# Kernel tuning notes

Hardware: AMD Instinct MI355X
Metric: run time of the kernel (lower is better)

Reference implementation:

```python
import jax, jax.numpy as jnp
import numpy as np

# Level-7 icosphere: nv vertices, nf faces
NV, NF = 163842, 327680
IN_C, NECK_C, OUT_C, B = 64, 32, 128, 2
EPS = 1e-5


def setup_inputs() -> dict:
    key = jax.random.key(0)
    ks = jax.random.split(key, 16)
    f32 = jnp.float32
    d = {}
    d['x'] = jax.random.normal(ks[0], (B, IN_C, NV), f32)
    # conv1 (1x1), bn1
    d['w1'] = jax.random.normal(ks[1], (NECK_C, IN_C), f32) * 0.05
    d['b1'] = jnp.zeros((NECK_C,), f32)
    d['gamma1'] = jnp.ones((NECK_C,), f32); d['beta1'] = jnp.zeros((NECK_C,), f32)
    # MeshConv: coeffs (out,in,4 taps: id, lap, grad_ew, grad_ns) + bias
    d['coeffs'] = jax.random.normal(ks[2], (NECK_C, NECK_C, 4), f32) * 0.05
    d['mc_bias'] = jnp.zeros((NECK_C,), f32)
    d['gamma2'] = jnp.ones((NECK_C,), f32); d['beta2'] = jnp.zeros((NECK_C,), f32)
    # conv3 (1x1), bn3
    d['w3'] = jax.random.normal(ks[3], (OUT_C, NECK_C), f32) * 0.05
    d['b3'] = jnp.zeros((OUT_C,), f32)
    d['gamma3'] = jnp.ones((OUT_C,), f32); d['beta3'] = jnp.zeros((OUT_C,), f32)
    # shortcut conv_ + bn_ (diff_chan since in!=out)
    d['wsc'] = jax.random.normal(ks[4], (OUT_C, IN_C), f32) * 0.05
    d['bsc'] = jnp.zeros((OUT_C,), f32)
    d['gammasc'] = jnp.ones((OUT_C,), f32); d['betasc'] = jnp.zeros((OUT_C,), f32)
    # sparse mesh operators (gather indices + values):
    # G: face gradient, 3 components per face from 3 face vertices
    d['idx_G'] = jax.random.randint(ks[5], (NF, 3), 0, NV, jnp.int32)
    d['vals_G'] = jax.random.normal(ks[6], (NF, 3, 3), f32) * 0.1
    # EW/NS tangent direction per face (3-vectors)
    d['EW'] = jax.random.normal(ks[7], (NF, 3), f32)
    d['NS'] = jax.random.normal(ks[8], (NF, 3), f32)
    # L: vertex laplacian, ~7 nnz per row
    d['idx_L'] = jax.random.randint(ks[9], (NV, 7), 0, NV, jnp.int32)
    d['vals_L'] = jax.random.normal(ks[10], (NV, 7), f32) * 0.1
    # F2V: face-to-vertex averaging, ~6 faces per vertex
    d['idx_F2V'] = jax.random.randint(ks[11], (NV, 6), 0, NF, jnp.int32)
    d['vals_F2V'] = jax.random.uniform(ks[12], (NV, 6), f32) / 6.0
    return d


def _bn(x, g, b):
    # training-mode BatchNorm1d over (batch, spatial), per channel
    m = x.mean(axis=(0, 2), keepdims=True)
    v = ((x - m) ** 2).mean(axis=(0, 2), keepdims=True)
    return g[None, :, None] * (x - m) * jax.lax.rsqrt(v + EPS) + b[None, :, None]


def _conv1x1(x, w, b):
    return jnp.einsum('oc,bcn->bon', w, x) + b[None, :, None]


def _mesh_conv(x, coeffs, bias, idx_G, vals_G, EW, NS, idx_L, vals_L, idx_F2V, vals_F2V):
    # laplacian: sparse matmul via gather  (B,C,NV)
    lap = jnp.einsum('bcnk,nk->bcn', x[:, :, idx_L], vals_L)
    # face gradient: (B,C,NF,3 components)
    grad_face = jnp.einsum('bcfj,fij->bcfi', x[:, :, idx_G], vals_G)
    g_ew = jnp.einsum('bcfi,fi->bcf', grad_face, EW)
    g_ns = jnp.einsum('bcfi,fi->bcf', grad_face, NS)
    # face -> vertex averaging
    gv_ew = jnp.einsum('bcnk,nk->bcn', g_ew[:, :, idx_F2V], vals_F2V)
    gv_ns = jnp.einsum('bcnk,nk->bcn', g_ns[:, :, idx_F2V], vals_F2V)
    feat = jnp.stack([x, lap, gv_ew, gv_ns], axis=-1)  # (B,C,NV,4)
    return jnp.einsum('bcnk,ock->bon', feat, coeffs) + bias[None, :, None]


def reference(x, w1, b1, gamma1, beta1, coeffs, mc_bias, gamma2, beta2,
              w3, b3, gamma3, beta3, wsc, bsc, gammasc, betasc,
              idx_G, vals_G, EW, NS, idx_L, vals_L, idx_F2V, vals_F2V):
    # shortcut branch (diff_chan)
    x2 = _bn(_conv1x1(x, wsc, bsc), gammasc, betasc)
    # main branch
    h = jax.nn.relu(_bn(_conv1x1(x, w1, b1), gamma1, beta1))
    h = _mesh_conv(h, coeffs, mc_bias, idx_G, vals_G, EW, NS, idx_L, vals_L, idx_F2V, vals_F2V)
    h = jax.nn.relu(_bn(h, gamma2, beta2))
    h = _bn(_conv1x1(h, w3, b3), gamma3, beta3)
    return jax.nn.relu(h + x2)
```

## Files before the change

kernel.cpp:

```cpp
#include <hip/hip_runtime.h>

#define NV   163842
#define NF   327680
#define BB   2
#define INC  64
#define NECK 32
#define OUTC 128
#define NT   (BB*NV)
#define EPSB 1e-5f

typedef unsigned short ushort_t;
typedef __attribute__((ext_vector_type(8))) short bf16x8;
typedef __attribute__((ext_vector_type(4))) float f32x4;

#define F_SX8  0
#define F_SS8  512
#define F_A1   33280
#define F_C1   33312
#define F_ASC  33344
#define F_CSC  33472
#define F_S2S  33600
#define F_S2Q  33632
#define F_A2   33664
#define F_C2   33696
#define F_SHR  33728
#define F_SS2  33760
#define F_A3   34784
#define F_C3   34912
#define F_CF   35040
#define STATN  35168
#define F_W1B  35200
#define F_CFB  36224
#define F_Y1   38272
#define F_H2   (F_Y1 + NT*16)
#define F_I18  (F_H2 + NT*16)
#define F_WEW  (F_I18 + NV*18)
#define F_WNS  (F_WEW + NV*18)
#define F_XB   (F_WNS + NV*18)

#define FSTR 136

__device__ __forceinline__ float bf2f(ushort_t u) {
    union { unsigned int i; float f; } x; x.i = ((unsigned int)u) << 16; return x.f;
}
__device__ __forceinline__ ushort_t f2bf(float f) {
    union { float f; unsigned int i; } x; x.f = f;
    unsigned int r = x.i + 0x7fffu + ((x.i >> 16) & 1u);
    return (ushort_t)(r >> 16);
}

__global__ __launch_bounds__(256) void k_xcvt(const float* __restrict__ x,
                                              float* __restrict__ ws,
                                              ushort_t* __restrict__ xb) {
    __shared__ float SSl[64 * 68 + 64];
    const int tid = threadIdx.x;
    const int w = tid >> 6, l = tid & 63;
    const int o16 = l & 15, kg = l >> 4;

    for (int i = tid; i < 64 * 68 + 64; i += 256) SSl[i] = 0.f;
    __syncthreads();

    f32x4 acc[10];
#pragma unroll
    for (int i = 0; i < 10; ++i) acc[i] = (f32x4){0.f, 0.f, 0.f, 0.f};
    f32x4 accS[4];
#pragma unroll
    for (int i = 0; i < 4; ++i) accS[i] = (f32x4){0.f, 0.f, 0.f, 0.f};

    bf16x8 onesf;
    {
        short ov = (o16 == 0) ? (short)0x3F80 : (short)0;
#pragma unroll
        for (int j = 0; j < 8; ++j) onesf[j] = ov;
    }

    const int NCHB = (NV + 63) >> 6;
    const int NW = gridDim.x * 4;
    for (int cid = blockIdx.x * 4 + w; cid < 2 * NCHB; cid += NW) {
        const int b = (cid >= NCHB) ? 1 : 0;
        const int tc = cid - b * NCHB;
        const int n0 = tc << 6;
        const float* xsrc = x + (size_t)b * 64 * NV;
        const bool full = (n0 + 64 <= NV);
        const int n = n0 + l;
        if (n < NV) {
            unsigned int pk[32];
#pragma unroll
            for (int c2 = 0; c2 < 32; ++c2) {
                float f0 = xsrc[(size_t)(2 * c2) * NV + n];
                float f1 = xsrc[(size_t)(2 * c2 + 1) * NV + n];
                pk[c2] = (unsigned int)f2bf(f0) | ((unsigned int)f2bf(f1) << 16);
            }
            ushort_t* row = xb + (size_t)(b * NV + n) * 64;
#pragma unroll
            for (int j = 0; j < 8; ++j) {
                uint4 q = make_uint4(pk[4 * j], pk[4 * j + 1], pk[4 * j + 2], pk[4 * j + 3]);
                *(uint4*)(row + j * 8) = q;
            }
        }
        bf16x8 fr[4][2];
#pragma unroll
        for (int mt = 0; mt < 4; ++mt) {
            const float* rp = xsrc + (size_t)(mt * 16 + o16) * NV + n0;
#pragma unroll
            for (int ks = 0; ks < 2; ++ks) {
                const int v0 = ks * 32 + kg * 8;
                float f[8];
                if (full) {
                    float4 q0 = *(const float4*)(rp + v0);
                    float4 q1 = *(const float4*)(rp + v0 + 4);
                    f[0] = q0.x; f[1] = q0.y; f[2] = q0.z; f[3] = q0.w;
                    f[4] = q1.x; f[5] = q1.y; f[6] = q1.z; f[7] = q1.w;
                } else {
#pragma unroll
                    for (int j = 0; j < 8; ++j)
                        f[j] = (n0 + v0 + j < NV) ? rp[v0 + j] : 0.f;
                }
                bf16x8 fb;
#pragma unroll
                for (int j = 0; j < 8; ++j) fb[j] = (short)f2bf(f[j]);
                fr[mt][ks] = fb;
            }
        }
#pragma unroll
        for (int ks = 0; ks < 2; ++ks) {
            int tt = 0;
#pragma unroll
            for (int mt = 0; mt < 4; ++mt) {
#pragma unroll
                for (int nt2 = 0; nt2 < 4; ++nt2) {
                    if (nt2 >= mt) {
                        acc[tt] = __builtin_amdgcn_mfma_f32_16x16x32_bf16(fr[mt][ks], fr[nt2][ks], acc[tt], 0, 0, 0);
                        ++tt;
                    }
                }
                accS[mt] = __builtin_amdgcn_mfma_f32_16x16x32_bf16(onesf, fr[mt][ks], accS[mt], 0, 0, 0);
            }
        }
    }
    {
        int tt = 0;
#pragma unroll
        for (int mt = 0; mt < 4; ++mt) {
#pragma unroll
            for (int nt2 = 0; nt2 < 4; ++nt2) {
                if (nt2 >= mt) {
#pragma unroll
                    for (int r = 0; r < 4; ++r) {
                        const int row = mt * 16 + kg * 4 + r;
                        const int col = nt2 * 16 + o16;
                        atomicAdd(&SSl[row * 68 + col], acc[tt][r]);
                    }
                    ++tt;
                }
            }
            if (kg == 0) atomicAdd(&SSl[64 * 68 + mt * 16 + o16], accS[mt][0]);
        }
    }
    __syncthreads();
    {
        float* SSg = ws + F_SS8 + (size_t)(blockIdx.x & 7) * 4096;
        for (int i = tid; i < 64 * 64; i += 256) {
            const int r = i >> 6, c = i & 63;
            if (c >= r) {
                float v = SSl[r * 68 + c];
                if (v != 0.f) atomicAdd(&SSg[r * 64 + c], v);
            }
        }
        if (tid < 64) atomicAdd(&ws[F_SX8 + (blockIdx.x & 7) * 64 + tid], SSl[64 * 68 + tid]);
    }
}

__global__ __launch_bounds__(256) void k_fold1(const float* __restrict__ w1,
                                               const float* __restrict__ g1,
                                               const float* __restrict__ be1,
                                               const float* __restrict__ wsc,
                                               const float* __restrict__ gsc,
                                               const float* __restrict__ besc,
                                               float* __restrict__ ws,
                                               ushort_t* __restrict__ w1b) {
    __shared__ float SSl[4096];
    __shared__ float Sxl[64];
    const int tid = threadIdx.x;
    for (int i = tid; i < 4096; i += 256) {
        const int r = i >> 6, c = i & 63;
        float v = 0.f;
        if (c >= r) {
#pragma unroll
            for (int s = 0; s < 8; ++s) v += ws[F_SS8 + s * 4096 + i];
        }
        SSl[i] = v;
    }
    if (tid < 64) {
        float v = 0.f;
#pragma unroll
        for (int s = 0; s < 8; ++s) v += ws[F_SX8 + s * 64 + tid];
        Sxl[tid] = v;
    }
    __syncthreads();
    for (int i = tid; i < 4096; i += 256) {
        const int r = i >> 6, c = i & 63;
        if (c < r) SSl[i] = SSl[c * 64 + r];
    }
    __syncthreads();
    if (tid >= 32) return;
    const int bk = blockIdx.x;
    const float* w;
    float gamma, beta;
    float *pa, *pc;
    if (bk == 0) {
        w = w1 + tid * 64; gamma = g1[tid]; beta = be1[tid];
        pa = ws + F_A1 + tid; pc = ws + F_C1 + tid;
    } else {
        int o = (bk - 1) * 32 + tid;
        w = wsc + o * 64; gamma = gsc[o]; beta = besc[o];
        pa = ws + F_ASC + o; pc = ws + F_CSC + o;
    }
    float4 wr[16];
#pragma unroll
    for (int i = 0; i < 16; ++i) wr[i] = *(const float4*)(w + i * 4);
    float dotm = 0.f, quad = 0.f;
#pragma unroll
    for (int i4 = 0; i4 < 16; ++i4) {
        float4 wi = wr[i4];
        float rd[4] = {0.f, 0.f, 0.f, 0.f};
#pragma unroll
        for (int j4 = 0; j4 < 16; ++j4) {
            float4 wj = wr[j4];
#pragma unroll
            for (int r = 0; r < 4; ++r) {
                const float* row = &SSl[(i4 * 4 + r) * 64 + j4 * 4];
                rd[r] += row[0] * wj.x + row[1] * wj.y + row[2] * wj.z + row[3] * wj.w;
            }
        }
        dotm += wi.x * Sxl[i4 * 4] + wi.y * Sxl[i4 * 4 + 1] + wi.z * Sxl[i4 * 4 + 2] + wi.w * Sxl[i4 * 4 + 3];
        quad += wi.x * rd[0] + wi.y * rd[1] + wi.z * rd[2] + wi.w * rd[3];
    }
    const float invN = 1.0f / (float)NT;
    const float mean0 = dotm * invN;
    const float var = quad * invN - mean0 * mean0;
    const float a = gamma * rsqrtf(var + EPSB);
    *pa = a;
    *pc = beta - a * mean0;
    if (bk == 0) {
#pragma unroll
        for (int i4 = 0; i4 < 16; ++i4) {
            w1b[tid * 64 + i4 * 4 + 0] = f2bf(a * wr[i4].x);
            w1b[tid * 64 + i4 * 4 + 1] = f2bf(a * wr[i4].y);
            w1b[tid * 64 + i4 * 4 + 2] = f2bf(a * wr[i4].z);
            w1b[tid * 64 + i4 * 4 + 3] = f2bf(a * wr[i4].w);
        }
    }
}

__global__ __launch_bounds__(256) void k_conv1(const ushort_t* __restrict__ xb,
                                               const ushort_t* __restrict__ w1b,
                                               const float* __restrict__ ws,
                                               ushort_t* __restrict__ y1) {
    const int tid = threadIdx.x;
    const int w = tid >> 6, l = tid & 63;
    const int o16 = l & 15, kg = l >> 4;
    bf16x8 af[2][2];
#pragma unroll
    for (int mt = 0; mt < 2; ++mt)
#pragma unroll
        for (int ks = 0; ks < 2; ++ks)
            af[mt][ks] = *(const bf16x8*)(w1b + (mt * 16 + o16) * 64 + ks * 32 + kg * 8);
    float c1r[2][4];
#pragma unroll
    for (int mt = 0; mt < 2; ++mt)
#pragma unroll
        for (int r = 0; r < 4; ++r)
            c1r[mt][r] = ws[F_C1 + mt * 16 + kg * 4 + r];

    const int NCH = (NT + 63) >> 6;
    for (int ch = blockIdx.x * 4 + w; ch < NCH; ch += gridDim.x * 4) {
        const int n0 = ch << 6;
        bf16x8 bf[4][2];
#pragma unroll
        for (int nt = 0; nt < 4; ++nt) {
            int row = n0 + nt * 16 + o16;
            row = row < NT ? row : NT - 1;
#pragma unroll
            for (int ks = 0; ks < 2; ++ks)
                bf[nt][ks] = *(const bf16x8*)(xb + (size_t)row * 64 + ks * 32 + kg * 8);
        }
        f32x4 acc[2][4];
#pragma unroll
        for (int mt = 0; mt < 2; ++mt)
#pragma unroll
            for (int nt = 0; nt < 4; ++nt) acc[mt][nt] = (f32x4){0.f, 0.f, 0.f, 0.f};
#pragma unroll
        for (int mt = 0; mt < 2; ++mt)
#pragma unroll
            for (int nt = 0; nt < 4; ++nt)
#pragma unroll
                for (int ks = 0; ks < 2; ++ks)
                    acc[mt][nt] = __builtin_amdgcn_mfma_f32_16x16x32_bf16(af[mt][ks], bf[nt][ks], acc[mt][nt], 0, 0, 0);
#pragma unroll
        for (int nt = 0; nt < 4; ++nt) {
            const int vert = n0 + nt * 16 + o16;
            if (vert < NT) {
#pragma unroll
                for (int mt = 0; mt < 2; ++mt) {
                    uint2 p;
                    p.x = (unsigned)f2bf(fmaxf(acc[mt][nt][0] + c1r[mt][0], 0.f)) |
                          ((unsigned)f2bf(fmaxf(acc[mt][nt][1] + c1r[mt][1], 0.f)) << 16);
                    p.y = (unsigned)f2bf(fmaxf(acc[mt][nt][2] + c1r[mt][2], 0.f)) |
                          ((unsigned)f2bf(fmaxf(acc[mt][nt][3] + c1r[mt][3], 0.f)) << 16);
                    *(uint2*)(y1 + (size_t)vert * 32 + mt * 16 + kg * 4) = p;
                }
            }
        }
    }
}

__global__ __launch_bounds__(256) void k_w18(const int* __restrict__ idx_F2V,
                                             const float* __restrict__ vals_F2V,
                                             const int* __restrict__ idx_G,
                                             const float* __restrict__ vals_G,
                                             const float* __restrict__ EW,
                                             const float* __restrict__ NS,
                                             int* __restrict__ i18,
                                             float* __restrict__ wew,
                                             float* __restrict__ wns) {
    const int n = blockIdx.x * 256 + threadIdx.x;
    if (n >= NV) return;
#pragma unroll
    for (int k = 0; k < 6; ++k) {
        int f = idx_F2V[n * 6 + k];
        float fv = vals_F2V[n * 6 + k];
        float e0 = EW[f * 3], e1 = EW[f * 3 + 1], e2 = EW[f * 3 + 2];
        float s0 = NS[f * 3], s1 = NS[f * 3 + 1], s2 = NS[f * 3 + 2];
#pragma unroll
        for (int j = 0; j < 3; ++j) {
            float g0 = vals_G[f * 9 + j], g1 = vals_G[f * 9 + 3 + j], g2 = vals_G[f * 9 + 6 + j];
            i18[n * 18 + k * 3 + j] = idx_G[f * 3 + j];
            wew[n * 18 + k * 3 + j] = fv * (g0 * e0 + g1 * e1 + g2 * e2);
            wns[n * 18 + k * 3 + j] = fv * (g0 * s0 + g1 * s1 + g2 * s2);
        }
    }
}

__global__ __launch_bounds__(256) void k_cvtcoef(const float* __restrict__ c,
                                                 ushort_t* __restrict__ cb) {
    int i = blockIdx.x * 256 + threadIdx.x;
    if (i < 4096) cb[i] = f2bf(c[i]);
}

__global__ __launch_bounds__(256, 3) void k_meshconv(const ushort_t* __restrict__ y1,
                                                     const ushort_t* __restrict__ cfb,
                                                     const int* __restrict__ idx_L,
                                                     const float* __restrict__ vals_L,
                                                     const int* __restrict__ i18,
                                                     const float* __restrict__ w18ew,
                                                     const float* __restrict__ w18ns,
                                                     ushort_t* __restrict__ h2,
                                                     float* __restrict__ ws) {
    __shared__ __align__(16) ushort_t feat[4][32 * FSTR];
    __shared__ float sred[64];
    const int tid = threadIdx.x;
    const int w = __builtin_amdgcn_readfirstlane(tid >> 6);
    const int lane = tid & 63;
    ushort_t* fw = &feat[w][0];
    const int bh = lane >> 5;
    const int c = lane & 31;
    const int ybase = bh * (NV * 32);
    const int o16 = lane & 15;
    const int kg = lane >> 4;

    if (tid < 64) sred[tid] = 0.f;
    __syncthreads();

    float ssum[8], sssq[8];
#pragma unroll
    for (int i = 0; i < 8; ++i) { ssum[i] = 0.f; sssq[i] = 0.f; }

    const int gw = blockIdx.x * 4 + w;
    const int NW = gridDim.x * 4;
    const int NCH = (NV + 15) >> 4;

    for (int ch = gw; ch < NCH; ch += NW) {
        const int n0 = ch << 4;
        for (int g = 0; g < 16; ++g) {
            const int n = n0 + g;
            const bool ok = (n < NV);
            const int nn = ok ? n : (NV - 1);
            float fx = bf2f(y1[ybase + (nn << 5) + c]);
            float lap = 0.f, gew = 0.f, gns = 0.f;
            const int* ilp = idx_L + nn * 7;
            const float* vlp = vals_L + nn * 7;
#pragma unroll
            for (int j = 0; j < 7; ++j) {
                int vi = ilp[j];
                float wv = vlp[j];
                lap += wv * bf2f(y1[ybase + (vi << 5) + c]);
            }
            const int* igp = i18 + nn * 18;
            const float* wep = w18ew + nn * 18;
            const float* wnp = w18ns + nn * 18;
#pragma unroll
            for (int j = 0; j < 18; ++j) {
                int vi = igp[j];
                float we = wep[j], wn = wnp[j];
                float v = bf2f(y1[ybase + (vi << 5) + c]);
                gew += we * v;
                gns += wn * v;
            }
            if (!ok) { fx = 0.f; lap = 0.f; gew = 0.f; gns = 0.f; }
            unsigned int lo = (unsigned int)f2bf(fx) | ((unsigned int)f2bf(lap) << 16);
            unsigned int hi = (unsigned int)f2bf(gew) | ((unsigned int)f2bf(gns) << 16);
            const int inst = bh * 16 + g;
            *(uint2*)(fw + inst * FSTR + (c << 2)) = make_uint2(lo, hi);
        }
        f32x4 acc[2][2];
#pragma unroll
        for (int mt = 0; mt < 2; ++mt)
#pragma unroll
            for (int nt = 0; nt < 2; ++nt) acc[mt][nt] = (f32x4){0.f, 0.f, 0.f, 0.f};
        bf16x8 bfr[2][4];
#pragma unroll
        for (int nt = 0; nt < 2; ++nt)
#pragma unroll
            for (int kt = 0; kt < 4; ++kt)
                bfr[nt][kt] = *(const bf16x8*)(fw + (nt * 16 + o16) * FSTR + kt * 32 + kg * 8);
#pragma unroll
        for (int mt = 0; mt < 2; ++mt) {
#pragma unroll
            for (int kt = 0; kt < 4; ++kt) {
                bf16x8 af = *(const bf16x8*)(cfb + (mt * 16 + o16) * 128 + kt * 32 + kg * 8);
                acc[mt][0] = __builtin_amdgcn_mfma_f32_16x16x32_bf16(af, bfr[0][kt], acc[mt][0], 0, 0, 0);
                acc[mt][1] = __builtin_amdgcn_mfma_f32_16x16x32_bf16(af, bfr[1][kt], acc[mt][1], 0, 0, 0);
            }
        }
        const int n = n0 + o16;
        if (n < NV) {
#pragma unroll
            for (int nt = 0; nt < 2; ++nt) {
                const int rowb = ((nt * NV + n) << 5);
#pragma unroll
                for (int mt = 0; mt < 2; ++mt) {
#pragma unroll
                    for (int r = 0; r < 4; ++r) {
                        float v = acc[mt][nt][r];
                        int o = mt * 16 + kg * 4 + r;
                        h2[rowb + o] = f2bf(v);
                        ssum[mt * 4 + r] += v;
                        sssq[mt * 4 + r] += v * v;
                    }
                }
            }
        }
    }

#pragma unroll
    for (int si = 0; si < 8; ++si) {
#pragma unroll
        for (int m = 1; m < 16; m <<= 1) {
            ssum[si] += __shfl_xor(ssum[si], m, 16);
            sssq[si] += __shfl_xor(sssq[si], m, 16);
        }
    }
    if (o16 == 0) {
#pragma unroll
        for (int mt = 0; mt < 2; ++mt)
#pragma unroll
            for (int r = 0; r < 4; ++r) {
                int o = mt * 16 + kg * 4 + r;
                atomicAdd(&sred[o], ssum[mt * 4 + r]);
                atomicAdd(&sred[32 + o], sssq[mt * 4 + r]);
            }
    }
    __syncthreads();
    if (tid < 64) atomicAdd(&ws[F_S2S + tid], sred[tid]);
}

__global__ void k_fold2(const float* __restrict__ g2, const float* __restrict__ be2,
                        float* __restrict__ ws) {
    const int c = threadIdx.x;
    if (c < 32) {
        const float invN = 1.0f / (float)NT;
        float m = ws[F_S2S + c] * invN;
        float var = ws[F_S2Q + c] * invN - m * m;
        float a = g2[c] * rsqrtf(var + EPSB);
        ws[F_A2 + c] = a;
        ws[F_C2 + c] = be2[c] - a * m;
    }
}

__global__ __launch_bounds__(256) void k_hrmoments(const ushort_t* __restrict__ h2,
                                                   float* __restrict__ ws) {
    __shared__ __align__(16) ushort_t tile[4][32 * 40];
    __shared__ float red[1056];
    const int tid = threadIdx.x;
    const int w = tid >> 6, l = tid & 63;
    ushort_t* T = &tile[w][0];
    const int c8 = (l & 3) * 8;
    const int v0 = l >> 2;
    const int fr = l & 15, kg = l >> 4;

    for (int i = tid; i < 1056; i += 256) red[i] = 0.f;
    __syncthreads();

    float a2r[8], c2r[8];
#pragma unroll
    for (int j = 0; j < 8; ++j) { a2r[j] = ws[F_A2 + c8 + j]; c2r[j] = ws[F_C2 + c8 + j]; }

    f32x4 acc[2][2];
#pragma unroll
    for (int a = 0; a < 2; ++a)
#pragma unroll
        for (int b = 0; b < 2; ++b) acc[a][b] = (f32x4){0.f, 0.f, 0.f, 0.f};
    float ssum[8];
#pragma unroll
    for (int j = 0; j < 8; ++j) ssum[j] = 0.f;

    const int NCH = (NT + 31) >> 5;
    for (int ch = blockIdx.x * 4 + w; ch < NCH; ch += gridDim.x * 4) {
        const int s0 = ch << 5;
#pragma unroll
        for (int i = 0; i < 2; ++i) {
            const int vert = i * 16 + v0;
            const int s = s0 + vert;
            uint4 q = make_uint4(0u, 0u, 0u, 0u);
            const bool ok = (s < NT);
            if (ok) q = *(const uint4*)(h2 + (size_t)s * 32 + c8);
            const ushort_t* qs = (const ushort_t*)&q;
            ushort_t hb[8];
#pragma unroll
            for (int j = 0; j < 8; ++j) {
                float hv = ok ? fmaxf(a2r[j] * bf2f(qs[j]) + c2r[j], 0.f) : 0.f;
                ssum[j] += hv;
                hb[j] = f2bf(hv);
            }
#pragma unroll
            for (int j = 0; j < 8; ++j) T[(c8 + j) * 40 + vert] = hb[j];
        }
        bf16x8 f0 = *(const bf16x8*)(T + fr * 40 + kg * 8);
        bf16x8 f1 = *(const bf16x8*)(T + (16 + fr) * 40 + kg * 8);
        acc[0][0] = __builtin_amdgcn_mfma_f32_16x16x32_bf16(f0, f0, acc[0][0], 0, 0, 0);
        acc[0][1] = __builtin_amdgcn_mfma_f32_16x16x32_bf16(f0, f1, acc[0][1], 0, 0, 0);
        acc[1][0] = __builtin_amdgcn_mfma_f32_16x16x32_bf16(f1, f0, acc[1][0], 0, 0, 0);
        acc[1][1] = __builtin_amdgcn_mfma_f32_16x16x32_bf16(f1, f1, acc[1][1], 0, 0, 0);
    }
#pragma unroll
    for (int mt = 0; mt < 2; ++mt)
#pragma unroll
        for (int nt = 0; nt < 2; ++nt)
#pragma unroll
            for (int r = 0; r < 4; ++r)
                atomicAdd(&red[(mt * 16 + kg * 4 + r) * 32 + nt * 16 + fr], acc[mt][nt][r]);
#pragma unroll
    for (int j = 0; j < 8; ++j) {
        float s = ssum[j];
        s += __shfl_xor(s, 4); s += __shfl_xor(s, 8);
        s += __shfl_xor(s, 16); s += __shfl_xor(s, 32);
        if (v0 == 0) atomicAdd(&red[1024 + c8 + j], s);
    }
    __syncthreads();
    for (int i = tid; i < 1024; i += 256) atomicAdd(&ws[F_SS2 + i], red[i]);
    if (tid < 32) atomicAdd(&ws[F_SHR + tid], red[1024 + tid]);
}

__global__ __launch_bounds__(128) void k_fold3(const float* __restrict__ w3,
                                               const float* __restrict__ wsc,
                                               const float* __restrict__ g3,
                                               const float* __restrict__ be3,
                                               float* __restrict__ ws,
                                               ushort_t* __restrict__ wfb) {
    __shared__ float SSl[1024];
    __shared__ float Sl[32];
    const int tid = threadIdx.x;
    for (int i = tid; i < 1024; i += 128) SSl[i] = ws[F_SS2 + i];
    if (tid < 32) Sl[tid] = ws[F_SHR + tid];
    __syncthreads();
    const int o = tid;
    float4 wr[8];
#pragma unroll
    for (int i = 0; i < 8; ++i) wr[i] = *(const float4*)(w3 + o * 32 + i * 4);
    float dotm = 0.f, quad = 0.f;
#pragma unroll
    for (int i4 = 0; i4 < 8; ++i4) {
        float4 wi = wr[i4];
        float rd[4] = {0.f, 0.f, 0.f, 0.f};
#pragma unroll
        for (int j4 = 0; j4 < 8; ++j4) {
            float4 wj = wr[j4];
#pragma unroll
            for (int r = 0; r < 4; ++r) {
                const float* row = &SSl[(i4 * 4 + r) * 32 + j4 * 4];
                rd[r] += row[0] * wj.x + row[1] * wj.y + row[2] * wj.z + row[3] * wj.w;
            }
        }
        dotm += wi.x * Sl[i4 * 4] + wi.y * Sl[i4 * 4 + 1] + wi.z * Sl[i4 * 4 + 2] + wi.w * Sl[i4 * 4 + 3];
        quad += wi.x * rd[0] + wi.y * rd[1] + wi.z * rd[2] + wi.w * rd[3];
    }
    const float invN = 1.0f / (float)NT;
    const float mean0 = dotm * invN;
    const float var = quad * invN - mean0 * mean0;
    const float a = g3[o] * rsqrtf(var + EPSB);
    const float cbias = be3[o] - a * mean0;
    ws[F_A3 + o] = a;
    ws[F_C3 + o] = cbias;
    const float asc = ws[F_ASC + o], csc = ws[F_CSC + o];
    ws[F_CF + o] = cbias + csc;
#pragma unroll
    for (int i4 = 0; i4 < 8; ++i4) {
        wfb[o * 96 + i4 * 4 + 0] = f2bf(a * wr[i4].x);
        wfb[o * 96 + i4 * 4 + 1] = f2bf(a * wr[i4].y);
        wfb[o * 96 + i4 * 4 + 2] = f2bf(a * wr[i4].z);
        wfb[o * 96 + i4 * 4 + 3] = f2bf(a * wr[i4].w);
    }
    for (int j = 0; j < 64; ++j)
        wfb[o * 96 + 32 + j] = f2bf(asc * wsc[o * 64 + j]);
}

__global__ __launch_bounds__(256) void k_final(const ushort_t* __restrict__ xb,
                                               const ushort_t* __restrict__ h2,
                                               const ushort_t* __restrict__ wfb,
                                               const float* __restrict__ ws,
                                               float* __restrict__ out) {
    __shared__ __align__(16) ushort_t feat[32 * 104];
    __shared__ __align__(16) float ol[128][33];
    const int tid = threadIdx.x;
    const int w = tid >> 6, l = tid & 63;
    const int fr = l & 15, kg = l >> 4;

    bf16x8 af[2][3];
#pragma unroll
    for (int mt = 0; mt < 2; ++mt)
#pragma unroll
        for (int kt = 0; kt < 3; ++kt)
            af[mt][kt] = *(const bf16x8*)(wfb + (w * 32 + mt * 16 + fr) * 96 + kt * 32 + kg * 8);
    float cfr[2][4];
#pragma unroll
    for (int mt = 0; mt < 2; ++mt)
#pragma unroll
        for (int r = 0; r < 4; ++r)
            cfr[mt][r] = ws[F_CF + w * 32 + mt * 16 + kg * 4 + r];

    const int hv = tid >> 3, hc4 = (tid & 7) * 4;
    float a2r[4], c2r[4];
#pragma unroll
    for (int j = 0; j < 4; ++j) { a2r[j] = ws[F_A2 + hc4 + j]; c2r[j] = ws[F_C2 + hc4 + j]; }
    const int xv = tid >> 3, xseg = tid & 7;
    const int oo = tid >> 1, ohalf = tid & 1;

    const int NCHK = (NV + 31) >> 5;
    for (int cid = blockIdx.x; cid < 2 * NCHK; cid += gridDim.x) {
        const int b = (cid >= NCHK) ? 1 : 0;
        const int t = cid - b * NCHK;
        const int n0 = t << 5;
        const int rem = NV - n0 < 32 ? NV - n0 : 32;
        {
            const int s = b * NV + n0 + hv;
            const bool ok = (hv < rem);
            uint2 q = make_uint2(0u, 0u);
            if (ok) q = *(const uint2*)(h2 + (size_t)s * 32 + hc4);
            const ushort_t* qs = (const ushort_t*)&q;
            unsigned int p0 = 0u, p1 = 0u;
            if (ok) {
                float h0 = fmaxf(a2r[0] * bf2f(qs[0]) + c2r[0], 0.f);
                float h1 = fmaxf(a2r[1] * bf2f(qs[1]) + c2r[1], 0.f);
                float h2v = fmaxf(a2r[2] * bf2f(qs[2]) + c2r[2], 0.f);
                float h3 = fmaxf(a2r[3] * bf2f(qs[3]) + c2r[3], 0.f);
                p0 = (unsigned int)f2bf(h0) | ((unsigned int)f2bf(h1) << 16);
                p1 = (unsigned int)f2bf(h2v) | ((unsigned int)f2bf(h3) << 16);
            }
            *(uint2*)(feat + hv * 104 + hc4) = make_uint2(p0, p1);
        }
        {
            const int s = b * NV + n0 + xv;
            uint4 q = make_uint4(0u, 0u, 0u, 0u);
            if (xv < rem) q = *(const uint4*)(xb + (size_t)s * 64 + xseg * 8);
            *(uint4*)(feat + xv * 104 + 32 + xseg * 8) = q;
        }
        __syncthreads();
        bf16x8 bf[2][3];
#pragma unroll
        for (int nt = 0; nt < 2; ++nt)
#pragma unroll
            for (int kt = 0; kt < 3; ++kt)
                bf[nt][kt] = *(const bf16x8*)(feat + (nt * 16 + fr) * 104 + kt * 32 + kg * 8);
        f32x4 acc[2][2];
#pragma unroll
        for (int mt = 0; mt < 2; ++mt)
#pragma unroll
            for (int nt = 0; nt < 2; ++nt) acc[mt][nt] = (f32x4){0.f, 0.f, 0.f, 0.f};
#pragma unroll
        for (int mt = 0; mt < 2; ++mt)
#pragma unroll
            for (int nt = 0; nt < 2; ++nt)
#pragma unroll
                for (int kt = 0; kt < 3; ++kt)
                    acc[mt][nt] = __builtin_amdgcn_mfma_f32_16x16x32_bf16(af[mt][kt], bf[nt][kt], acc[mt][nt], 0, 0, 0);
#pragma unroll
        for (int mt = 0; mt < 2; ++mt)
#pragma unroll
            for (int nt = 0; nt < 2; ++nt)
#pragma unroll
                for (int r = 0; r < 4; ++r)
                    ol[w * 32 + mt * 16 + kg * 4 + r][nt * 16 + fr] =
                        fmaxf(acc[mt][nt][r] + cfr[mt][r], 0.f);
        __syncthreads();
        {
            float* po = out + (size_t)(b * 128 + oo) * NV + n0 + ohalf * 16;
            if (rem == 32) {
#pragma unroll
                for (int j2 = 0; j2 < 8; ++j2)
                    *(float2*)(po + j2 * 2) = make_float2(ol[oo][ohalf * 16 + j2 * 2],
                                                         ol[oo][ohalf * 16 + j2 * 2 + 1]);
            } else {
#pragma unroll
                for (int j = 0; j < 16; ++j) {
                    int v = ohalf * 16 + j;
                    if (v < rem) po[j] = ol[oo][v];
                }
            }
        }
        __syncthreads();
    }
}

extern "C" void kernel_launch(void* const* d_in, const int* in_sizes, int n_in,
                              void* d_out, int out_size, void* d_ws, size_t ws_size,
                              hipStream_t stream) {
    (void)in_sizes; (void)n_in; (void)out_size; (void)ws_size;
    const float* x        = (const float*)d_in[0];
    const float* w1       = (const float*)d_in[1];
    const float* g1       = (const float*)d_in[3];
    const float* be1      = (const float*)d_in[4];
    const float* coeffs   = (const float*)d_in[5];
    const float* g2       = (const float*)d_in[7];
    const float* be2      = (const float*)d_in[8];
    const float* w3       = (const float*)d_in[9];
    const float* g3       = (const float*)d_in[11];
    const float* be3      = (const float*)d_in[12];
    const float* wsc      = (const float*)d_in[13];
    const float* gsc      = (const float*)d_in[15];
    const float* besc     = (const float*)d_in[16];
    const int*   idx_G    = (const int*)d_in[17];
    const float* vals_G   = (const float*)d_in[18];
    const float* EW       = (const float*)d_in[19];
    const float* NS       = (const float*)d_in[20];
    const int*   idx_L    = (const int*)d_in[21];
    const float* vals_L   = (const float*)d_in[22];
    const int*   idx_F2V  = (const int*)d_in[23];
    const float* vals_F2V = (const float*)d_in[24];
    float* ws  = (float*)d_ws;
    float* out = (float*)d_out;

    ushort_t* w1b = (ushort_t*)(ws + F_W1B);
    ushort_t* cfb = (ushort_t*)(ws + F_CFB);
    ushort_t* y1  = (ushort_t*)(ws + F_Y1);
    ushort_t* h2  = (ushort_t*)(ws + F_H2);
    ushort_t* xb  = (ushort_t*)(ws + F_XB);
    ushort_t* wfb = (ushort_t*)(ws + F_Y1);

    hipMemsetAsync(ws, 0, STATN * sizeof(float), stream);
    hipLaunchKernelGGL(k_xcvt, dim3(1280), dim3(256), 0, stream, x, ws, xb);
    hipLaunchKernelGGL(k_w18, dim3((NV + 255) / 256), dim3(256), 0, stream,
                       idx_F2V, vals_F2V, idx_G, vals_G, EW, NS,
                       (int*)(ws + F_I18), ws + F_WEW, ws + F_WNS);
    hipLaunchKernelGGL(k_cvtcoef, dim3(16), dim3(256), 0, stream, coeffs, cfb);
    hipLaunchKernelGGL(k_fold1, dim3(5), dim3(256), 0, stream, w1, g1, be1, wsc, gsc, besc, ws, w1b);
    hipLaunchKernelGGL(k_conv1, dim3(1280), dim3(256), 0, stream, xb, w1b, ws, y1);
    hipLaunchKernelGGL(k_meshconv, dim3(768), dim3(256), 0, stream,
                       y1, cfb, idx_L, vals_L,
                       (const int*)(ws + F_I18), ws + F_WEW, ws + F_WNS,
                       h2, ws);
    hipLaunchKernelGGL(k_fold2, dim3(1), dim3(32), 0, stream, g2, be2, ws);
    hipLaunchKernelGGL(k_hrmoments, dim3(1024), dim3(256), 0, stream, h2, ws);
    hipLaunchKernelGGL(k_fold3, dim3(1), dim3(128), 0, stream, w3, wsc, g3, be3, ws, wfb);
    hipLaunchKernelGGL(k_final, dim3(2048), dim3(256), 0, stream, xb, h2, wfb, ws, out);
}
```

Measured before the change: 552.7 us.

## Gather two channels per lane and two vertices per wave in meshconv

The meshconv gather loop now has each lane load a 32-bit pair of bf16 channels, with the two half-waves handling two different vertices at once. This halves the number of gather iterations per chunk and the number of load instructions issued. Launch bounds are raised to 4 blocks/SM and the grid is grown to 1024 blocks to add occupancy. In exchange each lane holds more accumulators and loads index/weight data for both vertices, which raises register pressure and redundant scalar loads.

```diff
diff --git a/kernel.cpp b/kernel.cpp
--- a/kernel.cpp
+++ b/kernel.cpp
@@ -348,7 +348,7 @@
     if (i < 4096) cb[i] = f2bf(c[i]);
 }
 
-__global__ __launch_bounds__(256, 3) void k_meshconv(const ushort_t* __restrict__ y1,
+__global__ __launch_bounds__(256, 4) void k_meshconv(const ushort_t* __restrict__ y1,
                                                      const ushort_t* __restrict__ cfb,
                                                      const int* __restrict__ idx_L,
                                                      const float* __restrict__ vals_L,
@@ -363,8 +363,9 @@
     const int w = __builtin_amdgcn_readfirstlane(tid >> 6);
     const int lane = tid & 63;
     ushort_t* fw = &feat[w][0];
-    const int bh = lane >> 5;
-    const int c = lane & 31;
+    const int gh = lane >> 5;
+    const int bh = (lane >> 4) & 1;
+    const int c2 = lane & 15;
     const int ybase = bh * (NV * 32);
     const int o16 = lane & 15;
     const int kg = lane >> 4;
@@ -382,36 +383,58 @@
 
     for (int ch = gw; ch < NCH; ch += NW) {
         const int n0 = ch << 4;
-        for (int g = 0; g < 16; ++g) {
-            const int n = n0 + g;
+        for (int jj = 0; jj < 8; ++jj) {
+            const int gA = 2 * jj;
+            const int nA = n0 + gA;
+            const int nB = nA + 1;
+            const int nnA = (nA < NV) ? nA : NV - 1;
+            const int nnB = (nB < NV) ? nB : NV - 1;
+            const int n = n0 + gA + gh;
             const bool ok = (n < NV);
-            const int nn = ok ? n : (NV - 1);
-            float fx = bf2f(y1[ybase + (nn << 5) + c]);
-            float lap = 0.f, gew = 0.f, gns = 0.f;
-            const int* ilp = idx_L + nn * 7;
-            const float* vlp = vals_L + nn * 7;
+            const int nn = gh ? nnB : nnA;
+            const ushort_t* yb = y1 + ybase;
+            unsigned int qs = *(const unsigned int*)(yb + (nn << 5) + (c2 << 1));
+            float fx0 = bf2f((ushort_t)(qs & 0xffffu));
+            float fx1 = bf2f((ushort_t)(qs >> 16));
+            float lap0 = 0.f, lap1 = 0.f, ge0 = 0.f, ge1 = 0.f, gn0 = 0.f, gn1 = 0.f;
 #pragma unroll
             for (int j = 0; j < 7; ++j) {
-                int vi = ilp[j];
-                float wv = vlp[j];
-                lap += wv * bf2f(y1[ybase + (vi << 5) + c]);
-            }
-            const int* igp = i18 + nn * 18;
-            const float* wep = w18ew + nn * 18;
-            const float* wnp = w18ns + nn * 18;
+                const int viA = idx_L[nnA * 7 + j];
+                const int viB = idx_L[nnB * 7 + j];
+                const float wvA = vals_L[nnA * 7 + j];
+                const float wvB = vals_L[nnB * 7 + j];
+                const int vi = gh ? viB : viA;
+                const float wv = gh ? wvB : wvA;
+                unsigned int q = *(const unsigned int*)(yb + (vi << 5) + (c2 << 1));
+                lap0 += wv * bf2f((ushort_t)(q & 0xffffu));
+                lap1 += wv * bf2f((ushort_t)(q >> 16));
+            }
 #pragma unroll
             for (int j = 0; j < 18; ++j) {
-                int vi = igp[j];
-                float we = wep[j], wn = wnp[j];
-                float v = bf2f(y1[ybase + (vi << 5) + c]);
-                gew += we * v;
-                gns += wn * v;
-            }
-            if (!ok) { fx = 0.f; lap = 0.f; gew = 0.f; gns = 0.f; }
-            unsigned int lo = (unsigned int)f2bf(fx) | ((unsigned int)f2bf(lap) << 16);
-            unsigned int hi = (unsigned int)f2bf(gew) | ((unsigned int)f2bf(gns) << 16);
-            const int inst = bh * 16 + g;
-            *(uint2*)(fw + inst * FSTR + (c << 2)) = make_uint2(lo, hi);
+                const int viA = i18[nnA * 18 + j];
+                const int viB = i18[nnB * 18 + j];
+                const float weA = w18ew[nnA * 18 + j];
+                const float weB = w18ew[nnB * 18 + j];
+                const float wnA = w18ns[nnA * 18 + j];
+                const float wnB = w18ns[nnB * 18 + j];
+                const int vi = gh ? viB : viA;
+                const float we = gh ? weB : weA;
+                const float wn = gh ? wnB : wnA;
+                unsigned int q = *(const unsigned int*)(yb + (vi << 5) + (c2 << 1));
+                float v0 = bf2f((ushort_t)(q & 0xffffu));
+                float v1 = bf2f((ushort_t)(q >> 16));
+                ge0 += we * v0; ge1 += we * v1;
+                gn0 += wn * v0; gn1 += wn * v1;
+            }
+            unsigned int u0 = 0u, u1 = 0u, u2 = 0u, u3 = 0u;
+            if (ok) {
+                u0 = (unsigned int)f2bf(fx0) | ((unsigned int)f2bf(lap0) << 16);
+                u1 = (unsigned int)f2bf(ge0) | ((unsigned int)f2bf(gn0) << 16);
+                u2 = (unsigned int)f2bf(fx1) | ((unsigned int)f2bf(lap1) << 16);
+                u3 = (unsigned int)f2bf(ge1) | ((unsigned int)f2bf(gn1) << 16);
+            }
+            const int inst = bh * 16 + gA + gh;
+            *(uint4*)(fw + inst * FSTR + (c2 << 3)) = make_uint4(u0, u1, u2, u3);
         }
         f32x4 acc[2][2];
 #pragma unroll
@@ -765,7 +788,7 @@
     hipLaunchKernelGGL(k_cvtcoef, dim3(16), dim3(256), 0, stream, coeffs, cfb);
     hipLaunchKernelGGL(k_fold1, dim3(5), dim3(256), 0, stream, w1, g1, be1, wsc, gsc, besc, ws, w1b);
     hipLaunchKernelGGL(k_conv1, dim3(1280), dim3(256), 0, stream, xb, w1b, ws, y1);
-    hipLaunchKernelGGL(k_meshconv, dim3(768), dim3(256), 0, stream,
+    hipLaunchKernelGGL(k_meshconv, dim3(1024), dim3(256), 0, stream,
                        y1, cfb, idx_L, vals_L,
                        (const int*)(ws + F_I18), ws + F_WEW, ws + F_WNS,
                        h2, ws);
```

Result: no change. 542.6 us (-1.8%).
